# Performance work log

Hardware: AMD Instinct MI355X
Metric: run time of the kernel (lower is better)

Reference implementation:

```python
import jax, jax.numpy as jnp
import numpy as np

N_NODES = 100000
N_EDGES = 3200000
F_IN = 256
H1 = 128   # growth_rate * bn_size
H2 = 32    # growth_rate
BN_EPS = 1e-5


def _gin_bn_relu(x, edge_index, Wa, ba, Wb, bb, gamma, beta):
    # GINConv (eps=0): h_i = MLP(x_i + sum_{j in N(i)} x_j)
    src, dst = edge_index[0], edge_index[1]
    agg = jax.ops.segment_sum(x[src], dst, num_segments=x.shape[0])  # [N, F]
    h = x + agg
    # nn1: Linear -> ReLU -> Linear
    h = jnp.maximum(h @ Wa + ba, 0.0)
    h = h @ Wb + bb
    # BatchNorm1d (training-mode batch stats over nodes)
    mean = h.mean(axis=0)
    var = h.var(axis=0)  # biased, matches torch BN normalization
    h = (h - mean) * jax.lax.rsqrt(var + BN_EPS) * gamma + beta
    return jnp.maximum(h, 0.0)


def setup_inputs() -> dict:
    key = jax.random.key(0)
    ks = jax.random.split(key, 12)
    x = jax.random.normal(ks[0], (N_NODES, F_IN), dtype=jnp.float32)
    edge_index = jax.random.randint(ks[1], (2, N_EDGES), 0, N_NODES, dtype=jnp.int64)

    def lin(k, fin, fout):
        s = 1.0 / np.sqrt(fin)
        return jax.random.uniform(k, (fin, fout), jnp.float32, -s, s)

    return {
        "x": x,
        "edge_index": edge_index,
        "W1a": lin(ks[2], F_IN, H1), "b1a": jnp.zeros((H1,), jnp.float32),
        "W1b": lin(ks[3], H1, H1),   "b1b": jnp.zeros((H1,), jnp.float32),
        "g1": jnp.ones((H1,), jnp.float32), "be1": jnp.zeros((H1,), jnp.float32),
        "W2a": lin(ks[4], H1, H2),   "b2a": jnp.zeros((H2,), jnp.float32),
        "W2b": lin(ks[5], H2, H2),   "b2b": jnp.zeros((H2,), jnp.float32),
        "g2": jnp.ones((H2,), jnp.float32), "be2": jnp.zeros((H2,), jnp.float32),
    }


def reference(x, edge_index, W1a, b1a, W1b, b1b, g1, be1,
              W2a, b2a, W2b, b2b, g2, be2):
    # data.x is a single tensor -> [x]; torch.cat([x], 1) == x (concat is a no-op)
    h = _gin_bn_relu(x, edge_index, W1a, b1a, W1b, b1b, g1, be1)   # [N, 128]
    h = _gin_bn_relu(h, edge_index, W2a, b2a, W2b, b2b, g2, be2)   # [N, 32]
    return h
```

## Files before the change

### kernel.cpp

```cpp
#include <hip/hip_runtime.h>

#define F_IN 256
#define H1 128
#define H2 32
#define BN_EPS 1e-5f
#define BSHIFT 8
#define BCAP 16384
#define CHUNK 2048
#define NSHARD 8

typedef short bf16x8 __attribute__((ext_vector_type(8)));
typedef float f32x4 __attribute__((ext_vector_type(4)));

__device__ __forceinline__ ushort f2bf(float f) {
    uint u = __float_as_uint(f);
    return (ushort)((u + 0x7FFFu + ((u >> 16) & 1u)) >> 16);
}
__device__ __forceinline__ float bf2f(ushort h) {
    return __uint_as_float((uint)h << 16);
}
__device__ __forceinline__ uint pack2(float a, float b) {
    return (uint)f2bf(a) | ((uint)f2bf(b) << 16);
}
__device__ __forceinline__ void unpack2(uint u, float& a, float& b) {
    a = __uint_as_float(u << 16);
    b = __uint_as_float(u & 0xFFFF0000u);
}
__device__ __forceinline__ int clampN(int v, int N) {
    return v < 0 ? 0 : (v >= N ? N - 1 : v);
}

__global__ __launch_bounds__(256) void super0_k(
    const float* __restrict__ W1a, const float* __restrict__ W1b,
    const float* __restrict__ W2a, const float* __restrict__ W2b,
    ushort* __restrict__ w1aT, ushort* __restrict__ w1bT,
    ushort* __restrict__ w2aT, ushort* __restrict__ w2bT,
    int* __restrict__ bucket_cursor, float* __restrict__ sums1,
    float* __restrict__ sums2) {
    const int tid = threadIdx.x;
    if (blockIdx.x == 212) {
        for (int i = tid; i < 512; i += 256) bucket_cursor[i] = 0;
        for (int i = tid; i < NSHARD * 2 * H1; i += 256) sums1[i] = 0.f;
        for (int i = tid; i < NSHARD * 2 * H2; i += 256) sums2[i] = 0.f;
        return;
    }
    int idx = blockIdx.x * 256 + tid;
    if (idx < 32768) {
        int k = idx >> 7, c = idx & 127;
        w1aT[c * 256 + k] = f2bf(W1a[idx]);
    } else if (idx < 49152) {
        int t = idx - 32768;
        int k = t >> 7, c = t & 127;
        w1bT[c * 128 + k] = f2bf(W1b[t]);
    } else if (idx < 53248) {
        int t = idx - 49152;
        int k = t >> 5, c = t & 31;
        w2aT[c * 128 + k] = f2bf(W2a[t]);
    } else if (idx < 54272) {
        int t = idx - 53248;
        int k = t >> 5, c = t & 31;
        w2bT[c * 32 + k] = f2bf(W2b[t]);
    }
}

__device__ __forceinline__ void binA_body(int bid, const int* __restrict__ eb,
                                          int E, int N, int NBUCK,
                                          int* __restrict__ bucket_cursor,
                                          uint* __restrict__ rec) {
    __shared__ int lcnt[512];
    __shared__ int lbase[512];
    __shared__ uint lrec[CHUNK];
    __shared__ ushort lbk[CHUNK];
    __shared__ ushort lrk[CHUNK];
    __shared__ int nzf;
    const int tid = threadIdx.x;
    const int cbase = bid * CHUNK;
    const int cnum = min(CHUNK, E - cbase);
    if (cnum <= 0) return;
    if (tid == 0) nzf = 0;
    __syncthreads();
    {
        int i = tid * (CHUNK / 256);
        if (i < cnum && eb[2 * (cbase + i) + 1] != 0) atomicAdd(&nzf, 1);
    }
    for (int i = tid; i < NBUCK; i += 256) lcnt[i] = 0;
    __syncthreads();
    const int is64 = (nzf == 0);
    for (int i = tid; i < cnum; i += 256) {
        int e = cbase + i;
        int s = is64 ? eb[2 * e] : eb[e];
        int d = is64 ? eb[2 * (E + e)] : eb[E + e];
        s = clampN(s, N);
        d = clampN(d, N);
        int bk = d >> BSHIFT;
        int rk = atomicAdd(&lcnt[bk], 1);
        lrec[i] = (uint)s | ((uint)(d & 255) << 17);
        lbk[i] = (ushort)bk;
        lrk[i] = (ushort)rk;
    }
    __syncthreads();
    for (int i = tid; i < NBUCK; i += 256)
        lbase[i] = atomicAdd(&bucket_cursor[i], lcnt[i]);
    __syncthreads();
    for (int i = tid; i < cnum; i += 256) {
        int bk = lbk[i];
        int pos = lbase[bk] + lrk[i];
        if (pos < BCAP) rec[(size_t)bk * BCAP + pos] = lrec[i];
    }
}

__device__ __forceinline__ void gemm1_body(int bid, const float* __restrict__ Af,
                                           const ushort* __restrict__ WT,
                                           ushort* __restrict__ outb, int N) {
    constexpr int K = F_IN, NC = H1, NF = NC / 16;
    const int lane = threadIdx.x & 63;
    const int wave = threadIdx.x >> 6;
    const int row0 = bid * 64 + wave * 16;
    const int col = lane & 15;
    const int k0 = (lane >> 4) * 8;
    int arow = row0 + col;
    if (arow >= N) arow = N - 1;

    f32x4 acc[NF];
#pragma unroll
    for (int f = 0; f < NF; ++f) acc[f] = (f32x4){0.f, 0.f, 0.f, 0.f};
#pragma unroll
    for (int kc = 0; kc < K; kc += 32) {
        const float* ap = &Af[(size_t)arow * K + kc + k0];
        float4 p = *(const float4*)ap;
        float4 q = *(const float4*)(ap + 4);
        bf16x8 af;
        af[0] = (short)f2bf(p.x); af[1] = (short)f2bf(p.y);
        af[2] = (short)f2bf(p.z); af[3] = (short)f2bf(p.w);
        af[4] = (short)f2bf(q.x); af[5] = (short)f2bf(q.y);
        af[6] = (short)f2bf(q.z); af[7] = (short)f2bf(q.w);
#pragma unroll
        for (int f = 0; f < NF; ++f) {
            bf16x8 bf = *(const bf16x8*)&WT[(size_t)(f * 16 + col) * K + kc + k0];
            acc[f] = __builtin_amdgcn_mfma_f32_16x16x32_bf16(af, bf, acc[f], 0, 0, 0);
        }
    }
    const int crow = row0 + (lane >> 4) * 4;
#pragma unroll
    for (int f = 0; f < NF; ++f) {
        const int c = f * 16 + col;
#pragma unroll
        for (int j = 0; j < 4; ++j) {
            int rr = crow + j;
            if (rr < N) outb[(size_t)rr * NC + c] = f2bf(acc[f][j]);
        }
    }
}

__global__ __launch_bounds__(256) void super1_k(
    const int* __restrict__ eb, int E, int N, int NBUCK, int GB,
    int* __restrict__ bucket_cursor, uint* __restrict__ rec,
    const float* __restrict__ x, const ushort* __restrict__ w1aT,
    ushort* __restrict__ t1b) {
    if ((int)blockIdx.x < GB)
        binA_body(blockIdx.x, eb, E, N, NBUCK, bucket_cursor, rec);
    else
        gemm1_body(blockIdx.x - GB, x, w1aT, t1b, N);
}

__global__ __launch_bounds__(256) void binB_k(const uint* __restrict__ rec,
                                              const int* __restrict__ bucket_cursor,
                                              int N, int NBUCK,
                                              int* __restrict__ row_start,
                                              int* __restrict__ esrc) {
    __shared__ int cntA[256];
    __shared__ int cntB[256];
    __shared__ int red[256];
    const int bk = blockIdx.x;
    const int tid = threadIdx.x;
    int part = 0;
    for (int i = tid; i < bk; i += 256) {
        int c = bucket_cursor[i];
        part += (c < BCAP) ? c : BCAP;
    }
    red[tid] = part;
    __syncthreads();
    for (int s = 128; s > 0; s >>= 1) {
        if (tid < s) red[tid] += red[tid + s];
        __syncthreads();
    }
    const int base = red[0];
    int cnt = bucket_cursor[bk];
    if (cnt > BCAP) cnt = BCAP;
    if (bk == NBUCK - 1 && tid == 0) row_start[N] = base + cnt;

    const uint* r = rec + (size_t)bk * BCAP;
    cntA[tid] = 0;
    __syncthreads();
    for (int i = tid; i < cnt; i += 256) atomicAdd(&cntA[r[i] >> 17], 1);
    __syncthreads();
    int* src = cntA;
    int* dst = cntB;
    for (int off = 1; off < 256; off <<= 1) {
        int v = src[tid] + (tid >= off ? src[tid - off] : 0);
        __syncthreads();
        dst[tid] = v;
        __syncthreads();
        int* t = src; src = dst; dst = t;
    }
    const int n0 = bk << BSHIFT;
    {
        int node = n0 + tid;
        if (node < N) row_start[node] = base + (tid ? src[tid - 1] : 0);
    }
    dst[tid] = 0;
    __syncthreads();
    for (int i = tid; i < cnt; i += 256) {
        uint rv = r[i];
        int dl = rv >> 17;
        int rank = atomicAdd(&dst[dl], 1);
        esrc[base + (dl ? src[dl - 1] : 0) + rank] = (int)(rv & 0x1FFFFu);
    }
}

template <int NC, bool BIAS, bool OUT_BF16, bool STATS, int NF>
__device__ __forceinline__ void gemm_epilogue(f32x4* acc, const float* bias,
                                              void* outv, int N, int row0,
                                              int lane, float* sums) {
    __shared__ float ssum[NC];
    __shared__ float ssq[NC];
    if (STATS) {
        if (threadIdx.x < NC) { ssum[threadIdx.x] = 0.f; ssq[threadIdx.x] = 0.f; }
        __syncthreads();
    }
    const int col0 = lane & 15;
    const int crow = row0 + (lane >> 4) * 4;
#pragma unroll
    for (int f = 0; f < NF; ++f) {
        const int c = f * 16 + col0;
        float bv = BIAS ? bias[c] : 0.f;
        float sv = 0.f, qv = 0.f;
#pragma unroll
        for (int j = 0; j < 4; ++j) {
            int rr = crow + j;
            if (rr < N) {
                float v = acc[f][j] + bv;
                if (OUT_BF16) ((ushort*)outv)[(size_t)rr * NC + c] = f2bf(v);
                else          ((float*)outv)[(size_t)rr * NC + c] = v;
                if (STATS) { sv += v; qv += v * v; }
            }
        }
        if (STATS) {
            sv += __shfl_xor(sv, 16); sv += __shfl_xor(sv, 32);
            qv += __shfl_xor(qv, 16); qv += __shfl_xor(qv, 32);
            if ((lane >> 4) == 0) {
                atomicAdd(&ssum[c], sv);
                atomicAdd(&ssq[c], qv);
            }
        }
    }
    if (STATS) {
        __syncthreads();
        if (threadIdx.x < NC) {
            float* sh = sums + (blockIdx.x & (NSHARD - 1)) * 2 * NC;
            atomicAdd(&sh[threadIdx.x], ssum[threadIdx.x]);
            atomicAdd(&sh[NC + threadIdx.x], ssq[threadIdx.x]);
        }
    }
}

template <int K, int NC, bool BIAS, bool OUT_BF16, bool STATS>
__global__ __launch_bounds__(256) void gemm_mfma_k(const ushort* __restrict__ A,
                                                   const ushort* __restrict__ WT,
                                                   const float* __restrict__ bias,
                                                   void* __restrict__ outv, int N,
                                                   float* __restrict__ sums) {
    constexpr int NF = NC / 16;
    const int lane = threadIdx.x & 63;
    const int wave = threadIdx.x >> 6;
    const int row0 = blockIdx.x * 64 + wave * 16;
    const int col = lane & 15;
    const int k0 = (lane >> 4) * 8;
    int arow = row0 + col;
    if (arow >= N) arow = N - 1;

    f32x4 acc[NF];
#pragma unroll
    for (int f = 0; f < NF; ++f) acc[f] = (f32x4){0.f, 0.f, 0.f, 0.f};
#pragma unroll
    for (int kc = 0; kc < K; kc += 32) {
        bf16x8 af = *(const bf16x8*)&A[(size_t)arow * K + kc + k0];
#pragma unroll
        for (int f = 0; f < NF; ++f) {
            bf16x8 bf = *(const bf16x8*)&WT[(size_t)(f * 16 + col) * K + kc + k0];
            acc[f] = __builtin_amdgcn_mfma_f32_16x16x32_bf16(af, bf, acc[f], 0, 0, 0);
        }
    }
    gemm_epilogue<NC, BIAS, OUT_BF16, STATS, NF>(acc, bias, outv, N, row0, lane, sums);
}

template <int K, int NC, bool OUT_BF16>
__global__ __launch_bounds__(256) void gemm_mfma_bnA_k(const ushort* __restrict__ U,
                                                       const ushort* __restrict__ WT,
                                                       const float* __restrict__ sums,
                                                       const float* __restrict__ g,
                                                       const float* __restrict__ be,
                                                       int Nbn,
                                                       void* __restrict__ outv, int N) {
    constexpr int NF = NC / 16;
    __shared__ __align__(16) float lsc[K];
    __shared__ __align__(16) float lsh[K];
    const int tid = threadIdx.x;
    if (tid < K) {
        float s = 0.f, q = 0.f;
#pragma unroll
        for (int sh = 0; sh < NSHARD; ++sh) {
            s += sums[sh * 2 * K + tid];
            q += sums[sh * 2 * K + K + tid];
        }
        float inv_n = 1.f / (float)Nbn;
        float mean = s * inv_n;
        float var = q * inv_n - mean * mean;
        float sc = g[tid] * rsqrtf(var + BN_EPS);
        lsc[tid] = sc;
        lsh[tid] = be[tid] - mean * sc;
    }
    __syncthreads();

    const int lane = tid & 63;
    const int wave = tid >> 6;
    const int row0 = blockIdx.x * 64 + wave * 16;
    const int col = lane & 15;
    const int k0 = (lane >> 4) * 8;
    int arow = row0 + col;
    if (arow >= N) arow = N - 1;

    f32x4 acc[NF];
#pragma unroll
    for (int f = 0; f < NF; ++f) acc[f] = (f32x4){0.f, 0.f, 0.f, 0.f};
#pragma unroll
    for (int kc = 0; kc < K; kc += 32) {
        bf16x8 raw = *(const bf16x8*)&U[(size_t)arow * K + kc + k0];
        float4 c0 = *(const float4*)&lsc[kc + k0];
        float4 c1 = *(const float4*)&lsc[kc + k0 + 4];
        float4 h0 = *(const float4*)&lsh[kc + k0];
        float4 h1 = *(const float4*)&lsh[kc + k0 + 4];
        bf16x8 af;
        af[0] = (short)f2bf(fmaxf(bf2f((ushort)raw[0]) * c0.x + h0.x, 0.f));
        af[1] = (short)f2bf(fmaxf(bf2f((ushort)raw[1]) * c0.y + h0.y, 0.f));
        af[2] = (short)f2bf(fmaxf(bf2f((ushort)raw[2]) * c0.z + h0.z, 0.f));
        af[3] = (short)f2bf(fmaxf(bf2f((ushort)raw[3]) * c0.w + h0.w, 0.f));
        af[4] = (short)f2bf(fmaxf(bf2f((ushort)raw[4]) * c1.x + h1.x, 0.f));
        af[5] = (short)f2bf(fmaxf(bf2f((ushort)raw[5]) * c1.y + h1.y, 0.f));
        af[6] = (short)f2bf(fmaxf(bf2f((ushort)raw[6]) * c1.z + h1.z, 0.f));
        af[7] = (short)f2bf(fmaxf(bf2f((ushort)raw[7]) * c1.w + h1.w, 0.f));
#pragma unroll
        for (int f = 0; f < NF; ++f) {
            bf16x8 bf = *(const bf16x8*)&WT[(size_t)(f * 16 + col) * K + kc + k0];
            acc[f] = __builtin_amdgcn_mfma_f32_16x16x32_bf16(af, bf, acc[f], 0, 0, 0);
        }
    }
    gemm_epilogue<NC, false, OUT_BF16, false, NF>(acc, nullptr, outv, N, row0, lane, nullptr);
}

__global__ void agg_f128b_k(const ushort* __restrict__ T, const int* __restrict__ row_start,
                            const int* __restrict__ esrc, const float* __restrict__ bias,
                            ushort* __restrict__ out, int N) {
    const int hw = (blockIdx.x << 3) | (threadIdx.x >> 5);
    const int lane = threadIdx.x & 31;
    if (hw >= N) return;
    const uint2* T2 = (const uint2*)T;
    uint2 sv = T2[(size_t)hw * 32 + lane];
    float a0, a1, a2, a3;
    unpack2(sv.x, a0, a1);
    unpack2(sv.y, a2, a3);
    int p = row_start[hw];
    const int pe = row_start[hw + 1];
    for (; p + 3 < pe; p += 4) {
        int s0 = esrc[p], s1 = esrc[p + 1], s2 = esrc[p + 2], s3 = esrc[p + 3];
        uint2 v0 = T2[(size_t)s0 * 32 + lane];
        uint2 v1 = T2[(size_t)s1 * 32 + lane];
        uint2 v2 = T2[(size_t)s2 * 32 + lane];
        uint2 v3 = T2[(size_t)s3 * 32 + lane];
        float x0, x1, x2, x3;
        unpack2(v0.x, x0, x1); unpack2(v0.y, x2, x3);
        a0 += x0; a1 += x1; a2 += x2; a3 += x3;
        unpack2(v1.x, x0, x1); unpack2(v1.y, x2, x3);
        a0 += x0; a1 += x1; a2 += x2; a3 += x3;
        unpack2(v2.x, x0, x1); unpack2(v2.y, x2, x3);
        a0 += x0; a1 += x1; a2 += x2; a3 += x3;
        unpack2(v3.x, x0, x1); unpack2(v3.y, x2, x3);
        a0 += x0; a1 += x1; a2 += x2; a3 += x3;
    }
    for (; p < pe; ++p) {
        uint2 v = T2[(size_t)esrc[p] * 32 + lane];
        float x0, x1, x2, x3;
        unpack2(v.x, x0, x1); unpack2(v.y, x2, x3);
        a0 += x0; a1 += x1; a2 += x2; a3 += x3;
    }
    const float4 b = ((const float4*)bias)[lane];
    a0 = fmaxf(a0 + b.x, 0.f);
    a1 = fmaxf(a1 + b.y, 0.f);
    a2 = fmaxf(a2 + b.z, 0.f);
    a3 = fmaxf(a3 + b.w, 0.f);
    ((uint2*)out)[(size_t)hw * 32 + lane] = make_uint2(pack2(a0, a1), pack2(a2, a3));
}

__global__ void agg_f32b_k(const ushort* __restrict__ T, const int* __restrict__ row_start,
                           const int* __restrict__ esrc, const float* __restrict__ bias,
                           ushort* __restrict__ out, int N) {
    const int wid = (blockIdx.x << 2) | (threadIdx.x >> 6);
    const int lane = threadIdx.x & 63;
    const int g = lane >> 3, l8 = lane & 7;
    if (wid >= N) return;
    const uint2* T2 = (const uint2*)T;
    float a0 = 0.f, a1 = 0.f, a2 = 0.f, a3 = 0.f;
    const int p0 = row_start[wid];
    const int pe = row_start[wid + 1];
    for (int p = p0 + g; p < pe; p += 8) {
        uint2 v = T2[(size_t)esrc[p] * 8 + l8];
        float x0, x1, x2, x3;
        unpack2(v.x, x0, x1); unpack2(v.y, x2, x3);
        a0 += x0; a1 += x1; a2 += x2; a3 += x3;
    }
#pragma unroll
    for (int off = 8; off < 64; off <<= 1) {
        a0 += __shfl_xor(a0, off);
        a1 += __shfl_xor(a1, off);
        a2 += __shfl_xor(a2, off);
        a3 += __shfl_xor(a3, off);
    }
    if (g == 0) {
        uint2 sv = T2[(size_t)wid * 8 + l8];
        float s0, s1, s2, s3;
        unpack2(sv.x, s0, s1); unpack2(sv.y, s2, s3);
        const float4 b = ((const float4*)bias)[l8];
        a0 = fmaxf(a0 + s0 + b.x, 0.f);
        a1 = fmaxf(a1 + s1 + b.y, 0.f);
        a2 = fmaxf(a2 + s2 + b.z, 0.f);
        a3 = fmaxf(a3 + s3 + b.w, 0.f);
        ((uint2*)out)[(size_t)wid * 8 + l8] = make_uint2(pack2(a0, a1), pack2(a2, a3));
    }
}

template <int F>
__global__ void bnapply_fin_k(const float* __restrict__ U, const float* __restrict__ sums,
                              const float* __restrict__ g, const float* __restrict__ be,
                              int Nbn, float* __restrict__ out, int total4) {
    __shared__ __align__(16) float lsc[F];
    __shared__ __align__(16) float lsh[F];
    const int tid = threadIdx.x;
    if (tid < F) {
        float s = 0.f, q = 0.f;
#pragma unroll
        for (int sh = 0; sh < NSHARD; ++sh) {
            s += sums[sh * 2 * F + tid];
            q += sums[sh * 2 * F + F + tid];
        }
        float inv_n = 1.f / (float)Nbn;
        float mean = s * inv_n;
        float var = q * inv_n - mean * mean;
        float sc = g[tid] * rsqrtf(var + BN_EPS);
        lsc[tid] = sc;
        lsh[tid] = be[tid] - mean * sc;
    }
    __syncthreads();
    const float4* U4 = (const float4*)U;
    float4* O4 = (float4*)out;
    const int stride = gridDim.x * blockDim.x;
    for (int i = blockIdx.x * blockDim.x + tid; i < total4; i += stride) {
        int c4 = (i % (F / 4)) * 4;
        float4 u = U4[i];
        float4 sc = *(const float4*)&lsc[c4];
        float4 sh = *(const float4*)&lsh[c4];
        float4 o;
        o.x = fmaxf(u.x * sc.x + sh.x, 0.f);
        o.y = fmaxf(u.y * sc.y + sh.y, 0.f);
        o.z = fmaxf(u.z * sc.z + sh.z, 0.f);
        o.w = fmaxf(u.w * sc.w + sh.w, 0.f);
        O4[i] = o;
    }
}

extern "C" void kernel_launch(void* const* d_in, const int* in_sizes, int n_in,
                              void* d_out, int out_size, void* d_ws, size_t ws_size,
                              hipStream_t stream) {
    const float* x   = (const float*)d_in[0];
    const int*   eb  = (const int*)d_in[1];
    const float* W1a = (const float*)d_in[2];
    const float* b1a = (const float*)d_in[3];
    const float* W1b = (const float*)d_in[4];
    const float* b1b = (const float*)d_in[5];
    const float* g1  = (const float*)d_in[6];
    const float* be1 = (const float*)d_in[7];
    const float* W2a = (const float*)d_in[8];
    const float* b2a = (const float*)d_in[9];
    const float* W2b = (const float*)d_in[10];
    const float* b2b = (const float*)d_in[11];
    const float* g2  = (const float*)d_in[12];
    const float* be2 = (const float*)d_in[13];
    float* out = (float*)d_out;

    const int N = in_sizes[0] / F_IN;
    const int E = in_sizes[1] / 2;
    const int NBUCK = (N + 255) >> BSHIFT;

    char* w = (char*)d_ws;
    size_t off = 0;
    auto alloc = [&](size_t bytes) -> void* {
        void* p = w + off;
        off = (off + bytes + 255) & ~(size_t)255;
        return p;
    };
    ushort* B0 = (ushort*)alloc((size_t)N * H1 * 2);
    ushort* B1 = (ushort*)alloc((size_t)N * H1 * 2);
    char*   B2 = (char*)alloc((size_t)N * H1 * 4);
    ushort* u1b = (ushort*)B2;
    float*  u2  = (float*)B2;

    int* row_start = (int*)alloc((size_t)(N + 1) * 4);
    int* esrc      = (int*)alloc((size_t)E * 4);
    uint* rec      = (uint*)alloc((size_t)NBUCK * BCAP * 4);
    int* bucket_cursor = (int*)alloc(512 * 4);
    ushort* w1aT = (ushort*)alloc(F_IN * H1 * 2);
    ushort* w1bT = (ushort*)alloc(H1 * H1 * 2);
    ushort* w2aT = (ushort*)alloc(H1 * H2 * 2);
    ushort* w2bT = (ushort*)alloc(H2 * H2 * 2);
    float* sums1 = (float*)alloc(NSHARD * 2 * H1 * 4);
    float* sums2 = (float*)alloc(NSHARD * 2 * H2 * 4);

    const int GB = (E + CHUNK - 1) / CHUNK;
    const int G1 = (N + 63) / 64;

    super0_k<<<213, 256, 0, stream>>>(W1a, W1b, W2a, W2b, w1aT, w1bT, w2aT, w2bT,
                                      bucket_cursor, sums1, sums2);
    super1_k<<<GB + G1, 256, 0, stream>>>(eb, E, N, NBUCK, GB, bucket_cursor, rec,
                                          x, w1aT, B1);
    binB_k<<<NBUCK, 256, 0, stream>>>(rec, bucket_cursor, N, NBUCK, row_start, esrc);
    agg_f128b_k<<<(N + 7) / 8, 256, 0, stream>>>(B1, row_start, esrc, b1a, B0, N);
    gemm_mfma_k<H1, H1, true, true, true><<<G1, 256, 0, stream>>>(B0, w1bT, b1b, u1b, N, sums1);
    gemm_mfma_bnA_k<H1, H2, true><<<G1, 256, 0, stream>>>(u1b, w2aT, sums1, g1, be1, N, B1, N);
    agg_f32b_k<<<(N + 3) / 4, 256, 0, stream>>>(B1, row_start, esrc, b2a, B0, N);
    gemm_mfma_k<H2, H2, true, false, true><<<G1, 256, 0, stream>>>(B0, w2bT, b2b, u2, N, sums2);
    bnapply_fin_k<H2><<<3125, 256, 0, stream>>>(u2, sums2, g2, be2, N, out, N * H2 / 4);
}
```

Baseline: 387.2 us.

## Split fused binning/GEMM kernel, double binning chunk, unroll aggregation gather by 8

Splits the combined binning-plus-first-GEMM kernel back into two separate launches. Each binning block now handles twice as many edges, and the per-bucket cursor atomic is skipped when the local count is zero. The 128-wide aggregation loop is unrolled to 8 neighbours per step so more gather loads are in flight. The goal is to cut global atomic traffic and raise memory parallelism, at the cost of losing the overlap between binning and GEMM that the fused kernel allowed, plus more shared memory per binning block.

After: 387.8 us. No clear change (+0.1%).

```diff
diff --git a/kernel.cpp b/kernel.cpp
--- a/kernel.cpp
+++ b/kernel.cpp
@@ -6,7 +6,7 @@
 #define BN_EPS 1e-5f
 #define BSHIFT 8
 #define BCAP 16384
-#define CHUNK 2048
+#define CHUNK 4096
 #define NSHARD 8
 
 typedef short bf16x8 __attribute__((ext_vector_type(8)));
@@ -63,10 +63,10 @@
     }
 }
 
-__device__ __forceinline__ void binA_body(int bid, const int* __restrict__ eb,
-                                          int E, int N, int NBUCK,
-                                          int* __restrict__ bucket_cursor,
-                                          uint* __restrict__ rec) {
+__global__ __launch_bounds__(256) void binA_k(const int* __restrict__ eb,
+                                              int E, int N, int NBUCK,
+                                              int* __restrict__ bucket_cursor,
+                                              uint* __restrict__ rec) {
     __shared__ int lcnt[512];
     __shared__ int lbase[512];
     __shared__ uint lrec[CHUNK];
@@ -74,7 +74,7 @@
     __shared__ ushort lrk[CHUNK];
     __shared__ int nzf;
     const int tid = threadIdx.x;
-    const int cbase = bid * CHUNK;
+    const int cbase = blockIdx.x * CHUNK;
     const int cnum = min(CHUNK, E - cbase);
     if (cnum <= 0) return;
     if (tid == 0) nzf = 0;
@@ -100,7 +100,7 @@
     }
     __syncthreads();
     for (int i = tid; i < NBUCK; i += 256)
-        lbase[i] = atomicAdd(&bucket_cursor[i], lcnt[i]);
+        if (lcnt[i]) lbase[i] = atomicAdd(&bucket_cursor[i], lcnt[i]);
     __syncthreads();
     for (int i = tid; i < cnum; i += 256) {
         int bk = lbk[i];
@@ -109,13 +109,13 @@
     }
 }
 
-__device__ __forceinline__ void gemm1_body(int bid, const float* __restrict__ Af,
-                                           const ushort* __restrict__ WT,
-                                           ushort* __restrict__ outb, int N) {
+__global__ __launch_bounds__(256) void gemm1_k(const float* __restrict__ Af,
+                                               const ushort* __restrict__ WT,
+                                               ushort* __restrict__ outb, int N) {
     constexpr int K = F_IN, NC = H1, NF = NC / 16;
     const int lane = threadIdx.x & 63;
     const int wave = threadIdx.x >> 6;
-    const int row0 = bid * 64 + wave * 16;
+    const int row0 = blockIdx.x * 64 + wave * 16;
     const int col = lane & 15;
     const int k0 = (lane >> 4) * 8;
     int arow = row0 + col;
@@ -150,17 +150,6 @@
             if (rr < N) outb[(size_t)rr * NC + c] = f2bf(acc[f][j]);
         }
     }
-}
-
-__global__ __launch_bounds__(256) void super1_k(
-    const int* __restrict__ eb, int E, int N, int NBUCK, int GB,
-    int* __restrict__ bucket_cursor, uint* __restrict__ rec,
-    const float* __restrict__ x, const ushort* __restrict__ w1aT,
-    ushort* __restrict__ t1b) {
-    if ((int)blockIdx.x < GB)
-        binA_body(blockIdx.x, eb, E, N, NBUCK, bucket_cursor, rec);
-    else
-        gemm1_body(blockIdx.x - GB, x, w1aT, t1b, N);
 }
 
 __global__ __launch_bounds__(256) void binB_k(const uint* __restrict__ rec,
@@ -371,12 +360,17 @@
     unpack2(sv.y, a2, a3);
     int p = row_start[hw];
     const int pe = row_start[hw + 1];
-    for (; p + 3 < pe; p += 4) {
-        int s0 = esrc[p], s1 = esrc[p + 1], s2 = esrc[p + 2], s3 = esrc[p + 3];
+    for (; p + 7 < pe; p += 8) {
+        int s0 = esrc[p],     s1 = esrc[p + 1], s2 = esrc[p + 2], s3 = esrc[p + 3];
+        int s4 = esrc[p + 4], s5 = esrc[p + 5], s6 = esrc[p + 6], s7 = esrc[p + 7];
         uint2 v0 = T2[(size_t)s0 * 32 + lane];
         uint2 v1 = T2[(size_t)s1 * 32 + lane];
         uint2 v2 = T2[(size_t)s2 * 32 + lane];
         uint2 v3 = T2[(size_t)s3 * 32 + lane];
+        uint2 v4 = T2[(size_t)s4 * 32 + lane];
+        uint2 v5 = T2[(size_t)s5 * 32 + lane];
+        uint2 v6 = T2[(size_t)s6 * 32 + lane];
+        uint2 v7 = T2[(size_t)s7 * 32 + lane];
         float x0, x1, x2, x3;
         unpack2(v0.x, x0, x1); unpack2(v0.y, x2, x3);
         a0 += x0; a1 += x1; a2 += x2; a3 += x3;
@@ -385,6 +379,14 @@
         unpack2(v2.x, x0, x1); unpack2(v2.y, x2, x3);
         a0 += x0; a1 += x1; a2 += x2; a3 += x3;
         unpack2(v3.x, x0, x1); unpack2(v3.y, x2, x3);
+        a0 += x0; a1 += x1; a2 += x2; a3 += x3;
+        unpack2(v4.x, x0, x1); unpack2(v4.y, x2, x3);
+        a0 += x0; a1 += x1; a2 += x2; a3 += x3;
+        unpack2(v5.x, x0, x1); unpack2(v5.y, x2, x3);
+        a0 += x0; a1 += x1; a2 += x2; a3 += x3;
+        unpack2(v6.x, x0, x1); unpack2(v6.y, x2, x3);
+        a0 += x0; a1 += x1; a2 += x2; a3 += x3;
+        unpack2(v7.x, x0, x1); unpack2(v7.y, x2, x3);
         a0 += x0; a1 += x1; a2 += x2; a3 += x3;
     }
     for (; p < pe; ++p) {
@@ -529,8 +531,8 @@
 
     super0_k<<<213, 256, 0, stream>>>(W1a, W1b, W2a, W2b, w1aT, w1bT, w2aT, w2bT,
                                       bucket_cursor, sums1, sums2);
-    super1_k<<<GB + G1, 256, 0, stream>>>(eb, E, N, NBUCK, GB, bucket_cursor, rec,
-                                          x, w1aT, B1);
+    binA_k<<<GB, 256, 0, stream>>>(eb, E, N, NBUCK, bucket_cursor, rec);
+    gemm1_k<<<G1, 256, 0, stream>>>(x, w1aT, B1, N);
     binB_k<<<NBUCK, 256, 0, stream>>>(rec, bucket_cursor, N, NBUCK, row_start, esrc);
     agg_f128b_k<<<(N + 7) / 8, 256, 0, stream>>>(B1, row_start, esrc, b1a, B0, N);
     gemm_mfma_k<H1, H1, true, true, true><<<G1, 256, 0, stream>>>(B0, w1bT, b1b, u1b, N, sums1);
```
